# Optimization experiments

Measured on AMD Instinct MI355X. Metric: run time of the kernel, lower is better.

## Reference

```python
import jax, jax.numpy as jnp
import numpy as np

N_NODES = 50000
N_EDGES = 800000
N_GRAPHS = 64
D = 96              # input_dim = hidden_dim = output_dim
N_GIN = 4           # num_layers - 1 GINConv layers
N_HEADS = 5         # num_layers linear_prediction heads
BN_EPS = 1e-5


def setup_inputs() -> dict:
    key = jax.random.key(0)
    ks = jax.random.split(key, 16)
    s = 1.0 / np.sqrt(D)
    h = jax.random.normal(ks[0], (N_NODES, D), dtype=jnp.float32)
    src = jax.random.randint(ks[1], (N_EDGES,), 0, N_NODES, dtype=jnp.int32)
    dst = jax.random.randint(ks[2], (N_EDGES,), 0, N_NODES, dtype=jnp.int32)
    # sorted node->graph ids; deterministic so every graph is non-empty
    graph_ids = (jnp.arange(N_NODES, dtype=jnp.int32) * N_GRAPHS) // N_NODES
    return {
        "h": h,
        # GIN layer MLPs (num_mlp_layers=2): Linear -> BN -> ReLU -> Linear
        "gin_W1": jax.random.uniform(ks[3], (N_GIN, D, D), jnp.float32, -s, s),
        "gin_b1": jax.random.uniform(ks[4], (N_GIN, D), jnp.float32, -s, s),
        "gin_bn1_g": jnp.ones((N_GIN, D), jnp.float32),
        "gin_bn1_b": jnp.zeros((N_GIN, D), jnp.float32),
        "gin_W2": jax.random.uniform(ks[5], (N_GIN, D, D), jnp.float32, -s, s),
        "gin_b2": jax.random.uniform(ks[6], (N_GIN, D), jnp.float32, -s, s),
        # per-layer outer BatchNorm1d
        "bn_g": jnp.ones((N_GIN, D), jnp.float32),
        "bn_b": jnp.zeros((N_GIN, D), jnp.float32),
        # shared PReLU parameter (nn.PReLU default: 1 param, init 0.25)
        "prelu_a": jnp.full((1,), 0.25, jnp.float32),
        # linear_prediction heads
        "lin_W": jax.random.uniform(ks[7], (N_HEADS, D, D), jnp.float32, -s, s),
        "lin_b": jax.random.uniform(ks[8], (N_HEADS, D), jnp.float32, -s, s),
        "src": src,
        "dst": dst,
        "graph_ids": graph_ids,
    }


def _batchnorm(x, gamma, beta):
    # training-mode batch statistics over the node dim (biased variance, as torch)
    m = jnp.mean(x, axis=0)
    v = jnp.var(x, axis=0)
    return gamma * (x - m) * jax.lax.rsqrt(v + BN_EPS) + beta


def reference(h, gin_W1, gin_b1, gin_bn1_g, gin_bn1_b, gin_W2, gin_b2,
              bn_g, bn_b, prelu_a, lin_W, lin_b, src, dst, graph_ids):
    hidden_rep = [h]
    for l in range(N_GIN):
        # GINConv, sum aggregation, eps=0 (learn_eps=False): (1+eps)*h + sum_{j in N(i)} h_j
        agg = jax.ops.segment_sum(h[src], dst, num_segments=N_NODES)  # [N, D]
        z = h + agg
        # apply_func MLP: Linear -> BN -> ReLU -> Linear
        z = jax.nn.relu(_batchnorm(z @ gin_W1[l] + gin_b1[l], gin_bn1_g[l], gin_bn1_b[l]))
        z = z @ gin_W2[l] + gin_b2[l]
        # outer BatchNorm + PReLU
        z = _batchnorm(z, bn_g[l], bn_b[l])
        h = jnp.where(z >= 0, z, prelu_a * z)
        hidden_rep.append(h)
    # max graph pooling + per-layer linear heads (dropout = identity in eval)
    reps = []
    for l, hr in enumerate(hidden_rep):
        pooled = jax.ops.segment_max(hr, graph_ids, num_segments=N_GRAPHS)  # [B, D]
        reps.append(pooled @ lin_W[l] + lin_b[l])
    # layer_aggregation='cat': stack on dim=-1 then flatten -> [B, D * (N_GIN+1)]
    return jnp.stack(reps, axis=-1).reshape(N_GRAPHS, -1)
```

## Files before the change

### kernel.cpp

```cpp
#include <hip/hip_runtime.h>
#include <hip/hip_bf16.h>

#define N_NODES 50000
#define N_EDGES 800000
#define N_GRAPHS 64
#define D 96
#define N_GIN 4
#define BN_EPS 1e-5f
#define PCH 64
#define SC_PASSES 7
#define SC_SHIFT 13
#define SC_BLOCKS 1024
#define GEMM_GRID 782
#define LP 104
#define CPAD 16
#define ELLCAP 64

typedef __bf16 bf16;
typedef __bf16 bf16x8 __attribute__((ext_vector_type(8)));
typedef float f32x4 __attribute__((ext_vector_type(4)));
typedef unsigned short u16;

__device__ inline unsigned enc(float f) {
    unsigned b = __float_as_uint(f);
    return (b & 0x80000000u) ? ~b : (b | 0x80000000u);
}
__device__ inline float dec(unsigned u) {
    return __uint_as_float((u & 0x80000000u) ? (u ^ 0x80000000u) : ~u);
}

__global__ void k_prolog(const float* __restrict__ h, bf16* __restrict__ hb,
                         const float* __restrict__ W1, const float* __restrict__ W2,
                         bf16* __restrict__ wf, int* __restrict__ cnt,
                         float* __restrict__ stats, unsigned* __restrict__ pooledu) {
    int b = blockIdx.x;
    int tid = threadIdx.x;
    if (b < 2344) {
        int e = (b * 256 + tid) * 8;
        if (e >= N_NODES * D) return;
        float4 v0 = *(const float4*)(h + e);
        float4 v1 = *(const float4*)(h + e + 4);
        bf16x8 o;
        o[0] = (bf16)v0.x; o[1] = (bf16)v0.y; o[2] = (bf16)v0.z; o[3] = (bf16)v0.w;
        o[4] = (bf16)v1.x; o[5] = (bf16)v1.y; o[6] = (bf16)v1.z; o[7] = (bf16)v1.w;
        *(bf16x8*)(hb + e) = o;
    } else if (b < 2352) {
        int mat = b - 2344;
        const float* src = (mat < 4) ? (W1 + mat * D * D) : (W2 + (mat - 4) * D * D);
        bf16* dst = wf + mat * D * D;
        for (int p = tid; p < D * D; p += 256) {
            int f = p >> 9;
            int r = p & 511;
            int lane = r >> 3;
            int j = r & 7;
            int q = lane >> 4;
            int m16 = lane & 15;
            int nt = f / 3, ks = f % 3;
            int k = ks * 32 + q * 8 + j;
            int n = nt * 16 + m16;
            dst[p] = (bf16)src[k * D + n];
        }
    } else {
        int t = (b - 2352) * 256 + tid;
        if (t < N_NODES) cnt[(size_t)t * CPAD] = 0;
        if (t < N_GIN * 2 * 2 * D) stats[t] = 0.0f;
        if (t < 5 * N_GRAPHS * D) pooledu[t] = 0u;
    }
}

__global__ void __launch_bounds__(256) k_scatter_pool(
        const int* __restrict__ src, const int* __restrict__ dst,
        int* __restrict__ cnt, u16* __restrict__ ell,
        const bf16* __restrict__ hb, unsigned* __restrict__ pooledu) {
    if (blockIdx.x < SC_BLOCKS) {
        int tid = blockIdx.x * blockDim.x + threadIdx.x;
        int stride = SC_BLOCKS * blockDim.x;
        for (int p = 0; p < SC_PASSES; ++p) {
            for (int e = tid; e < N_EDGES; e += stride) {
                int d = dst[e];
                if ((d >> SC_SHIFT) == p) {
                    int pos = atomicAdd(&cnt[(size_t)d * CPAD], 1);
                    if (pos < ELLCAP) ell[(size_t)d * ELLCAP + pos] = (u16)src[e];
                }
            }
        }
    } else {
        int grp = (blockIdx.x - SC_BLOCKS) * 16 + (threadIdx.x >> 4);
        int l = threadIdx.x & 15;
        if (l >= 12) return;
        int g = grp / PCH, c = grp % PCH;
        int gs = (g * N_NODES + N_GRAPHS - 1) / N_GRAPHS;
        int ge = ((g + 1) * N_NODES + N_GRAPHS - 1) / N_GRAPHS;
        int len = ge - gs;
        int rs = gs + (len * c) / PCH;
        int re = gs + (len * (c + 1)) / PCH;
        const bf16x8* __restrict__ base = (const bf16x8*)hb;
        float m[8];
#pragma unroll
        for (int j = 0; j < 8; ++j) m[j] = -3e38f;
        int i = rs;
        for (; i + 2 <= re; i += 2) {
            bf16x8 r0 = base[i * 12 + l];
            bf16x8 r1 = base[(i + 1) * 12 + l];
#pragma unroll
            for (int j = 0; j < 8; ++j) m[j] = fmaxf(m[j], fmaxf((float)r0[j], (float)r1[j]));
        }
        if (i < re) {
            bf16x8 r = base[i * 12 + l];
#pragma unroll
            for (int j = 0; j < 8; ++j) m[j] = fmaxf(m[j], (float)r[j]);
        }
        unsigned* dstp = pooledu + (size_t)g * D + l * 8;
#pragma unroll
        for (int j = 0; j < 8; ++j) atomicMax(&dstp[j], enc(m[j]));
    }
}

__global__ void __launch_bounds__(256) k_agg_gemm(
        const bf16* __restrict__ prev, const int* __restrict__ cnt,
        const u16* __restrict__ ell, const bf16* __restrict__ Bf,
        const float* __restrict__ bias, bf16* __restrict__ Z,
        float* __restrict__ ssum, float* __restrict__ sssq) {
    __shared__ bf16 sA[4][16 * LP];
    __shared__ float sr1[4][D], sr2[4][D];
    int tid = threadIdx.x;
    int lane = tid & 63, wv = tid >> 6;
    int q = lane >> 4, m16 = lane & 15;
    int strip = blockIdx.x * 4 + wv;

    float psum[6], pssq[6];
#pragma unroll
    for (int f = 0; f < 6; ++f) { psum[f] = 0.0f; pssq[f] = 0.0f; }

    if (strip < 3125) {
        const bf16x8* __restrict__ base = (const bf16x8*)prev;
        int grp = q, gl = m16;
#pragma unroll 1
        for (int r = 0; r < 4; ++r) {
            int node = strip * 16 + r * 4 + grp;
            if (gl < 12) {
                float acc[8];
                bf16x8 self = base[node * 12 + gl];
#pragma unroll
                for (int j = 0; j < 8; ++j) acc[j] = (float)self[j];
                int dg = cnt[(size_t)node * CPAD];
                if (dg > ELLCAP) dg = ELLCAP;
                const u16* ep = ell + (size_t)node * ELLCAP;
                int e = 0;
                for (; e + 8 <= dg; e += 8) {
                    int s0 = ep[e];
                    int s1 = ep[e + 1];
                    int s2 = ep[e + 2];
                    int s3 = ep[e + 3];
                    int s4 = ep[e + 4];
                    int s5 = ep[e + 5];
                    int s6 = ep[e + 6];
                    int s7 = ep[e + 7];
                    bf16x8 r0 = base[s0 * 12 + gl];
                    bf16x8 r1 = base[s1 * 12 + gl];
                    bf16x8 r2 = base[s2 * 12 + gl];
                    bf16x8 r3 = base[s3 * 12 + gl];
                    bf16x8 r4 = base[s4 * 12 + gl];
                    bf16x8 r5 = base[s5 * 12 + gl];
                    bf16x8 r6 = base[s6 * 12 + gl];
                    bf16x8 r7 = base[s7 * 12 + gl];
#pragma unroll
                    for (int j = 0; j < 8; ++j) {
                        acc[j] += (float)r0[j] + (float)r1[j] + (float)r2[j] + (float)r3[j]
                                + (float)r4[j] + (float)r5[j] + (float)r6[j] + (float)r7[j];
                    }
                }
                for (; e < dg; ++e) {
                    int s = ep[e];
                    bf16x8 rr = base[s * 12 + gl];
#pragma unroll
                    for (int j = 0; j < 8; ++j) acc[j] += (float)rr[j];
                }
                bf16x8 o;
#pragma unroll
                for (int j = 0; j < 8; ++j) o[j] = (bf16)acc[j];
                *(bf16x8*)&sA[wv][(r * 4 + grp) * LP + gl * 8] = o;
            }
        }
        __asm__ volatile("s_waitcnt lgkmcnt(0)" ::: "memory");

        bf16x8 bfr[18];
#pragma unroll
        for (int f = 0; f < 18; ++f) bfr[f] = *(const bf16x8*)(Bf + (f * 64 + lane) * 8);

        bf16x8 a0 = *(const bf16x8*)&sA[wv][m16 * LP + q * 8];
        bf16x8 a1 = *(const bf16x8*)&sA[wv][m16 * LP + 32 + q * 8];
        bf16x8 a2 = *(const bf16x8*)&sA[wv][m16 * LP + 64 + q * 8];

#pragma unroll
        for (int f = 0; f < 6; ++f) {
            f32x4 acc = {0.0f, 0.0f, 0.0f, 0.0f};
            acc = __builtin_amdgcn_mfma_f32_16x16x32_bf16(a0, bfr[f * 3 + 0], acc, 0, 0, 0);
            acc = __builtin_amdgcn_mfma_f32_16x16x32_bf16(a1, bfr[f * 3 + 1], acc, 0, 0, 0);
            acc = __builtin_amdgcn_mfma_f32_16x16x32_bf16(a2, bfr[f * 3 + 2], acc, 0, 0, 0);
            int col = f * 16 + m16;
            float bvf = bias[col];
            bf16* zp = Z + (size_t)(strip * 16 + q * 4) * D + col;
#pragma unroll
            for (int i = 0; i < 4; ++i) {
                float v = acc[i] + bvf;
                zp[(size_t)i * D] = (bf16)v;
                psum[f] += v;
                pssq[f] += v * v;
            }
        }
    }
#pragma unroll
    for (int f = 0; f < 6; ++f) {
        float r = psum[f];
        r += __shfl_xor(r, 16);
        r += __shfl_xor(r, 32);
        float r2 = pssq[f];
        r2 += __shfl_xor(r2, 16);
        r2 += __shfl_xor(r2, 32);
        if (lane < 16) {
            sr1[wv][f * 16 + lane] = r;
            sr2[wv][f * 16 + lane] = r2;
        }
    }
    __syncthreads();
    int t = wv * 64 + lane;
    if (t < D) {
        atomicAdd(&ssum[t], sr1[0][t] + sr1[1][t] + sr1[2][t] + sr1[3][t]);
    } else if (t < 2 * D) {
        int u = t - D;
        atomicAdd(&sssq[u], sr2[0][u] + sr2[1][u] + sr2[2][u] + sr2[3][u]);
    }
}

__global__ void k_transform(const bf16* __restrict__ Z, const float* __restrict__ st,
                            const float* __restrict__ gamma, const float* __restrict__ beta,
                            const float* __restrict__ pa, bf16* __restrict__ O) {
    __shared__ float cs[D], ct[D];
    int t = threadIdx.x;
    if (t < D) {
        float m = st[t] * (1.0f / N_NODES);
        float v = st[D + t] * (1.0f / N_NODES) - m * m;
        float inv = rsqrtf(v + BN_EPS);
        float sc = gamma[t] * inv;
        cs[t] = sc;
        ct[t] = beta[t] - m * sc;
    }
    __syncthreads();
    int e = (blockIdx.x * 256 + t) * 8;
    if (e >= N_NODES * D) return;
    float alpha = pa[0];
    int c = e % D;
    bf16x8 z = *(const bf16x8*)(Z + e);
    bf16x8 o;
#pragma unroll
    for (int j = 0; j < 8; ++j) {
        float v = (float)z[j] * cs[c + j] + ct[c + j];
        o[j] = (bf16)(v >= 0.0f ? v : alpha * v);
    }
    *(bf16x8*)(O + e) = o;
}

__global__ void __launch_bounds__(256) k_gemm_fused(
        const bf16* __restrict__ A, const bf16* __restrict__ Bf,
        const float* __restrict__ st, const float* __restrict__ gamma,
        const float* __restrict__ beta, const float* __restrict__ bias,
        bf16* __restrict__ Z, float* __restrict__ ssum, float* __restrict__ sssq,
        unsigned* __restrict__ poolu) {
    __shared__ float cs[D], ct[D];
    __shared__ float sr1[4][D];
    __shared__ float sr2[4][D];
    __shared__ unsigned pmax[2 * D];
    int tid = threadIdx.x;
    if (tid < D) {
        float m = st[tid] * (1.0f / N_NODES);
        float v = st[D + tid] * (1.0f / N_NODES) - m * m;
        float inv = rsqrtf(v + BN_EPS);
        float sc = gamma[tid] * inv;
        cs[tid] = sc;
        ct[tid] = beta[tid] - m * sc;
    }
    if (tid < 2 * D) pmax[tid] = 0u;
    __syncthreads();

    int lane = tid & 63;
    int wv = tid >> 6;
    int w = (blockIdx.x * blockDim.x + tid) >> 6;
    int nw = (gridDim.x * blockDim.x) >> 6;
    int q = lane >> 4, m16 = lane & 15;
    int g0 = (int)(((long long)blockIdx.x * 64) * N_GRAPHS / N_NODES);

    float as_[3][8], at_[3][8];
#pragma unroll
    for (int ks = 0; ks < 3; ++ks)
#pragma unroll
        for (int j = 0; j < 8; ++j) {
            as_[ks][j] = cs[ks * 32 + q * 8 + j];
            at_[ks][j] = ct[ks * 32 + q * 8 + j];
        }

    bf16x8 bfr[18];
#pragma unroll
    for (int f = 0; f < 18; ++f) bfr[f] = *(const bf16x8*)(Bf + (f * 64 + lane) * 8);
    float bv[6];
#pragma unroll
    for (int f = 0; f < 6; ++f) bv[f] = bias[f * 16 + m16];
    float psum[6], pssq[6];
#pragma unroll
    for (int f = 0; f < 6; ++f) { psum[f] = 0.0f; pssq[f] = 0.0f; }

    const int NSTRIP = N_NODES / 16;
    for (int s = w; s < NSTRIP; s += nw) {
        const bf16* arow = A + (size_t)(s * 16 + m16) * D;
        bf16x8 z0 = *(const bf16x8*)(arow + q * 8);
        bf16x8 z1 = *(const bf16x8*)(arow + 32 + q * 8);
        bf16x8 z2 = *(const bf16x8*)(arow + 64 + q * 8);
        bf16x8 a0, a1, a2;
#pragma unroll
        for (int j = 0; j < 8; ++j) {
            a0[j] = (bf16)fmaxf(0.0f, (float)z0[j] * as_[0][j] + at_[0][j]);
            a1[j] = (bf16)fmaxf(0.0f, (float)z1[j] * as_[1][j] + at_[1][j]);
            a2[j] = (bf16)fmaxf(0.0f, (float)z2[j] * as_[2][j] + at_[2][j]);
        }
#pragma unroll
        for (int f = 0; f < 6; ++f) {
            f32x4 acc = {0.0f, 0.0f, 0.0f, 0.0f};
            acc = __builtin_amdgcn_mfma_f32_16x16x32_bf16(a0, bfr[f * 3 + 0], acc, 0, 0, 0);
            acc = __builtin_amdgcn_mfma_f32_16x16x32_bf16(a1, bfr[f * 3 + 1], acc, 0, 0, 0);
            acc = __builtin_amdgcn_mfma_f32_16x16x32_bf16(a2, bfr[f * 3 + 2], acc, 0, 0, 0);
            int col = f * 16 + m16;
            bf16* zp = Z + (size_t)(s * 16 + q * 4) * D + col;
#pragma unroll
            for (int i = 0; i < 4; ++i) {
                float v = acc[i] + bv[f];
                zp[(size_t)i * D] = (bf16)v;
                psum[f] += v;
                pssq[f] += v * v;
                int row = s * 16 + q * 4 + i;
                int g = (int)(((unsigned)row * 64u) / 50000u);
                int slot = g - g0;
                if (slot >= 0 && slot < 2)
                    atomicMax(&pmax[slot * D + col], enc(v));
            }
        }
    }
#pragma unroll
    for (int f = 0; f < 6; ++f) {
        float r = psum[f];
        r += __shfl_xor(r, 16);
        r += __shfl_xor(r, 32);
        float r2 = pssq[f];
        r2 += __shfl_xor(r2, 16);
        r2 += __shfl_xor(r2, 32);
        if (lane < 16) {
            sr1[wv][f * 16 + lane] = r;
            sr2[wv][f * 16 + lane] = r2;
        }
    }
    __syncthreads();
    int t = wv * 64 + lane;
    if (t < D) {
        atomicAdd(&ssum[t], sr1[0][t] + sr1[1][t] + sr1[2][t] + sr1[3][t]);
    } else if (t < 2 * D) {
        int u = t - D;
        atomicAdd(&sssq[u], sr2[0][u] + sr2[1][u] + sr2[2][u] + sr2[3][u]);
    }
    if (t < 2 * D) {
        int sl = t / D, c = t % D;
        int gg = g0 + sl;
        if (gg < N_GRAPHS && pmax[t] != 0u)
            atomicMax(&poolu[gg * D + c], pmax[t]);
    }
}

__global__ void k_heads(const unsigned* __restrict__ pooledu, const float* __restrict__ stats,
                        const float* __restrict__ bng, const float* __restrict__ bnb,
                        const float* __restrict__ pa, const float* __restrict__ W,
                        const float* __restrict__ B, float* __restrict__ out) {
    __shared__ float pv[D];
    int b = blockIdx.x;
    int l = b >> 6;
    int g = b & 63;
    int d = threadIdx.x;
    if (d < D) {
        float m = dec(pooledu[(size_t)(l * N_GRAPHS + g) * D + d]);
        if (l > 0) {
            int gl = l - 1;
            const float* st = stats + (gl * 2 + 1) * 2 * D;
            float mean = st[d] * (1.0f / N_NODES);
            float var = st[D + d] * (1.0f / N_NODES) - mean * mean;
            float inv = rsqrtf(var + BN_EPS);
            float s = bng[gl * D + d] * inv;
            float t = bnb[gl * D + d] - mean * s;
            float v = m * s + t;
            m = (v >= 0.0f) ? v : pa[0] * v;
        }
        pv[d] = m;
    }
    __syncthreads();
    if (d >= D) return;
    const float* w = W + (size_t)l * D * D;
    float acc = B[l * D + d];
    for (int k = 0; k < D; ++k) acc += pv[k] * w[k * D + d];
    out[g * (5 * D) + d * 5 + l] = acc;
}

extern "C" void kernel_launch(void* const* d_in, const int* in_sizes, int n_in,
                              void* d_out, int out_size, void* d_ws, size_t ws_size,
                              hipStream_t stream) {
    const float* h     = (const float*)d_in[0];
    const float* gW1   = (const float*)d_in[1];
    const float* gb1   = (const float*)d_in[2];
    const float* bn1g  = (const float*)d_in[3];
    const float* bn1b  = (const float*)d_in[4];
    const float* gW2   = (const float*)d_in[5];
    const float* gb2   = (const float*)d_in[6];
    const float* bng   = (const float*)d_in[7];
    const float* bnb   = (const float*)d_in[8];
    const float* prelu = (const float*)d_in[9];
    const float* linW  = (const float*)d_in[10];
    const float* linb  = (const float*)d_in[11];
    const int*   srcv  = (const int*)d_in[12];
    const int*   dstv  = (const int*)d_in[13];
    float* out = (float*)d_out;

    char* base = (char*)d_ws;
    size_t off = 0;
    auto carve = [&](size_t bytes) -> void* {
        void* p = base + off;
        off += (bytes + 255) & ~(size_t)255;
        return p;
    };
    const size_t HB = (size_t)N_NODES * D;
    bf16* hb0   = (bf16*)carve(HB * 2);
    bf16* hb1   = (bf16*)carve(HB * 2);
    bf16* zb    = (bf16*)carve(HB * 2);
    bf16* ab    = (bf16*)carve(HB * 2);
    bf16* wf    = (bf16*)carve(8 * D * D * 2);
    float* stats = (float*)carve(N_GIN * 2 * 2 * D * 4);
    int* cnt    = (int*)carve((size_t)N_NODES * CPAD * 4);
    u16* ell    = (u16*)carve((size_t)N_NODES * ELLCAP * 2);
    unsigned* pooledu = (unsigned*)carve(5 * N_GRAPHS * D * 4);

    k_prolog<<<2548, 256, 0, stream>>>(h, hb0, gW1, gW2, wf, cnt, stats, pooledu);
    k_scatter_pool<<<SC_BLOCKS + N_GRAPHS * PCH / 16, 256, 0, stream>>>(
        srcv, dstv, cnt, ell, hb0, pooledu);

    const bf16* prev = hb0;
    for (int l = 0; l < N_GIN; ++l) {
        float* st1 = stats + (l * 2 + 0) * 2 * D;
        float* st2 = stats + (l * 2 + 1) * 2 * D;
        if (l > 0) {
            float* stp = stats + ((l - 1) * 2 + 1) * 2 * D;
            k_transform<<<2344, 256, 0, stream>>>(ab, stp, bng + (l - 1) * D,
                                                  bnb + (l - 1) * D, prelu, hb1);
            prev = hb1;
        }
        k_agg_gemm<<<GEMM_GRID, 256, 0, stream>>>(prev, cnt, ell, wf + l * D * D,
                                                  gb1 + l * D, zb, st1, st1 + D);
        k_gemm_fused<<<GEMM_GRID, 256, 0, stream>>>(zb, wf + (4 + l) * D * D, st1,
                                                    bn1g + l * D, bn1b + l * D,
                                                    gb2 + l * D, ab, st2, st2 + D,
                                                    pooledu + (size_t)(l + 1) * N_GRAPHS * D);
    }
    k_heads<<<5 * N_GRAPHS, 128, 0, stream>>>(pooledu, stats, bng, bnb, prelu,
                                              linW, linb, out);
}
```

Baseline: 482.1 us.

## Build ELL adjacency via two-phase bucketed partition instead of global atomics

Replaces the multi-pass global-atomic scatter into the ELL table with a two-phase build. First, each block histograms and partitions its edge chunk by destination bucket in shared memory. Then one block per 256-node bucket assembles its rows in LDS and writes them out coalesced. This removes contended global atomics and the repeated passes over the edge list, at the cost of an extra kernel launch and an intermediate edge buffer. The count array is also un-padded and no longer zeroed in the prolog.

```diff
diff --git a/kernel.cpp b/kernel.cpp
--- a/kernel.cpp
+++ b/kernel.cpp
@@ -8,18 +8,22 @@
 #define N_GIN 4
 #define BN_EPS 1e-5f
 #define PCH 64
-#define SC_PASSES 7
-#define SC_SHIFT 13
-#define SC_BLOCKS 1024
 #define GEMM_GRID 782
 #define LP 104
-#define CPAD 16
 #define ELLCAP 64
+
+#define P1_BLOCKS 256
+#define EPB 3125
+#define BSH 8
+#define BNODES 256
+#define NBUCK 196
+#define SPITCH 33
 
 typedef __bf16 bf16;
 typedef __bf16 bf16x8 __attribute__((ext_vector_type(8)));
 typedef float f32x4 __attribute__((ext_vector_type(4)));
 typedef unsigned short u16;
+typedef unsigned int u32;
 
 __device__ inline unsigned enc(float f) {
     unsigned b = __float_as_uint(f);
@@ -31,8 +35,8 @@
 
 __global__ void k_prolog(const float* __restrict__ h, bf16* __restrict__ hb,
                          const float* __restrict__ W1, const float* __restrict__ W2,
-                         bf16* __restrict__ wf, int* __restrict__ cnt,
-                         float* __restrict__ stats, unsigned* __restrict__ pooledu) {
+                         bf16* __restrict__ wf, float* __restrict__ stats,
+                         unsigned* __restrict__ pooledu) {
     int b = blockIdx.x;
     int tid = threadIdx.x;
     if (b < 2344) {
@@ -62,31 +66,52 @@
         }
     } else {
         int t = (b - 2352) * 256 + tid;
-        if (t < N_NODES) cnt[(size_t)t * CPAD] = 0;
         if (t < N_GIN * 2 * 2 * D) stats[t] = 0.0f;
         if (t < 5 * N_GRAPHS * D) pooledu[t] = 0u;
     }
 }
 
-__global__ void __launch_bounds__(256) k_scatter_pool(
+__global__ void __launch_bounds__(256) k_part_pool(
         const int* __restrict__ src, const int* __restrict__ dst,
-        int* __restrict__ cnt, u16* __restrict__ ell,
+        u32* __restrict__ eo, u16* __restrict__ offs,
         const bf16* __restrict__ hb, unsigned* __restrict__ pooledu) {
-    if (blockIdx.x < SC_BLOCKS) {
-        int tid = blockIdx.x * blockDim.x + threadIdx.x;
-        int stride = SC_BLOCKS * blockDim.x;
-        for (int p = 0; p < SC_PASSES; ++p) {
-            for (int e = tid; e < N_EDGES; e += stride) {
-                int d = dst[e];
-                if ((d >> SC_SHIFT) == p) {
-                    int pos = atomicAdd(&cnt[(size_t)d * CPAD], 1);
-                    if (pos < ELLCAP) ell[(size_t)d * ELLCAP + pos] = (u16)src[e];
-                }
-            }
+    __shared__ u16 sdst[EPB + 3];
+    __shared__ u16 ssrc[EPB + 3];
+    __shared__ int hist[256];
+    __shared__ int incl[256];
+    int tid = threadIdx.x;
+    if (blockIdx.x < P1_BLOCKS) {
+        int e0 = blockIdx.x * EPB;
+        hist[tid] = 0;
+        __syncthreads();
+        for (int i = tid; i < EPB; i += 256) {
+            int d = dst[e0 + i];
+            sdst[i] = (u16)d;
+            ssrc[i] = (u16)src[e0 + i];
+            atomicAdd(&hist[d >> BSH], 1);
+        }
+        __syncthreads();
+        int v = hist[tid];
+        incl[tid] = v;
+        __syncthreads();
+        for (int o = 1; o < 256; o <<= 1) {
+            int t = (tid >= o) ? incl[tid - o] : 0;
+            __syncthreads();
+            incl[tid] += t;
+            __syncthreads();
+        }
+        int ex = incl[tid] - v;
+        if (tid <= NBUCK) offs[tid * P1_BLOCKS + blockIdx.x] = (u16)ex;
+        hist[tid] = ex;
+        __syncthreads();
+        for (int i = tid; i < EPB; i += 256) {
+            int d = sdst[i];
+            int pos = atomicAdd(&hist[d >> BSH], 1);
+            eo[e0 + pos] = ((u32)(d & (BNODES - 1)) << 16) | (u32)ssrc[i];
         }
     } else {
-        int grp = (blockIdx.x - SC_BLOCKS) * 16 + (threadIdx.x >> 4);
-        int l = threadIdx.x & 15;
+        int grp = (blockIdx.x - P1_BLOCKS) * 16 + (tid >> 4);
+        int l = tid & 15;
         if (l >= 12) return;
         int g = grp / PCH, c = grp % PCH;
         int gs = (g * N_NODES + N_GRAPHS - 1) / N_GRAPHS;
@@ -113,6 +138,35 @@
         unsigned* dstp = pooledu + (size_t)g * D + l * 8;
 #pragma unroll
         for (int j = 0; j < 8; ++j) atomicMax(&dstp[j], enc(m[j]));
+    }
+}
+
+__global__ void __launch_bounds__(256) k_ell_build(
+        const u32* __restrict__ eo, const u16* __restrict__ offs,
+        u16* __restrict__ ell, int* __restrict__ cnt) {
+    __shared__ u32 sell32[BNODES * SPITCH];
+    __shared__ int scnt[BNODES];
+    int tid = threadIdx.x;
+    int b = blockIdx.x;
+    scnt[tid] = 0;
+    __syncthreads();
+    int beg = offs[b * P1_BLOCKS + tid];
+    int end = offs[(b + 1) * P1_BLOCKS + tid];
+    const u32* ep = eo + (size_t)tid * EPB;
+    u16* srows = (u16*)sell32;
+    for (int i = beg; i < end; ++i) {
+        u32 pk = ep[i];
+        int dl = pk >> 16;
+        int pos = atomicAdd(&scnt[dl], 1);
+        if (pos < ELLCAP) srows[dl * (2 * SPITCH) + pos] = (u16)pk;
+    }
+    __syncthreads();
+    int node0 = b << BSH;
+    int nn = min(BNODES, N_NODES - node0);
+    if (tid < nn) cnt[node0 + tid] = scnt[tid];
+    u32* gell = (u32*)(ell + (size_t)node0 * ELLCAP);
+    for (int i = tid; i < nn * 32; i += 256) {
+        gell[i] = sell32[(i >> 5) * SPITCH + (i & 31)];
     }
 }
 
@@ -143,7 +197,7 @@
                 bf16x8 self = base[node * 12 + gl];
 #pragma unroll
                 for (int j = 0; j < 8; ++j) acc[j] = (float)self[j];
-                int dg = cnt[(size_t)node * CPAD];
+                int dg = cnt[node];
                 if (dg > ELLCAP) dg = ELLCAP;
                 const u16* ep = ell + (size_t)node * ELLCAP;
                 int e = 0;
@@ -438,13 +492,16 @@
     bf16* ab    = (bf16*)carve(HB * 2);
     bf16* wf    = (bf16*)carve(8 * D * D * 2);
     float* stats = (float*)carve(N_GIN * 2 * 2 * D * 4);
-    int* cnt    = (int*)carve((size_t)N_NODES * CPAD * 4);
+    int* cnt    = (int*)carve((size_t)N_NODES * 4);
     u16* ell    = (u16*)carve((size_t)N_NODES * ELLCAP * 2);
+    u32* eo     = (u32*)carve((size_t)N_EDGES * 4);
+    u16* offs   = (u16*)carve((size_t)(NBUCK + 1) * P1_BLOCKS * 2);
     unsigned* pooledu = (unsigned*)carve(5 * N_GRAPHS * D * 4);
 
-    k_prolog<<<2548, 256, 0, stream>>>(h, hb0, gW1, gW2, wf, cnt, stats, pooledu);
-    k_scatter_pool<<<SC_BLOCKS + N_GRAPHS * PCH / 16, 256, 0, stream>>>(
-        srcv, dstv, cnt, ell, hb0, pooledu);
+    k_prolog<<<2472, 256, 0, stream>>>(h, hb0, gW1, gW2, wf, stats, pooledu);
+    k_part_pool<<<P1_BLOCKS + N_GRAPHS * PCH / 16, 256, 0, stream>>>(
+        srcv, dstv, eo, offs, hb0, pooledu);
+    k_ell_build<<<NBUCK, 256, 0, stream>>>(eo, offs, ell, cnt);
 
     const bf16* prev = hb0;
     for (int l = 0; l < N_GIN; ++l) {
```

New measurement: 458.0 us. 1.05x faster.
